# Performance work log

Hardware: AMD Instinct MI355X
Metric: run time of the kernel (lower is better)

## Reference

```python
import jax, jax.numpy as jnp
import numpy as np

BIT = 8
QMAX = 2 ** (BIT - 1) - 1          # 127
QMIN = -(2 ** (BIT - 1))           # -128
BOUNDARY_RANGE = 0.005
EPS = 1e-5


def _quant_act_int8(x):
    # StatsQ per-tensor activation quantization: scale from (1 - boundary_range)
    # quantile of |x| (robust absmax), fake-quant with STE.
    amax = jnp.maximum(jnp.quantile(jnp.abs(x), 1.0 - BOUNDARY_RANGE), EPS)
    s = QMAX / amax
    q = jnp.clip(jnp.round(x * s), QMIN, QMAX) / s
    return x + jax.lax.stop_gradient(q - x)


def _quant_w_ternary(w):
    # BitNet-1.58-style per-tensor ternary weight quantization:
    # gamma = mean(|W|); W_q in {-1, 0, +1} * gamma; STE.
    gamma = jnp.mean(jnp.abs(w)) + EPS
    q = jnp.clip(jnp.round(w / gamma), -1.0, 1.0) * gamma
    return w + jax.lax.stop_gradient(q - w)


def _qlinear(x, w):
    # quantize activations (int8 fake-quant) and weights (ternary), then matmul
    xq = _quant_act_int8(x)
    wq = _quant_w_ternary(w)
    return jnp.einsum('btd,hd->bth', xq, wq)


def _layernorm(x, g, b):
    mu = jnp.mean(x, axis=-1, keepdims=True)
    var = jnp.mean(jnp.square(x - mu), axis=-1, keepdims=True)
    return (x - mu) * jax.lax.rsqrt(var + 1e-5) * g + b


def setup_inputs() -> dict:
    key = jax.random.key(0)
    k_x, k_w1, k_w2 = jax.random.split(key, 3)
    B, T, D, H = 64, 256, 1024, 4096
    x = jax.random.normal(k_x, (B, T, D), dtype=jnp.float32)
    ln_g = jnp.ones((D,), dtype=jnp.float32)
    ln_b = jnp.zeros((D,), dtype=jnp.float32)
    w1 = jax.random.normal(k_w1, (H, D), dtype=jnp.float32) * (1.0 / np.sqrt(D))
    w2 = jax.random.normal(k_w2, (D, H), dtype=jnp.float32) * (1.0 / np.sqrt(H))
    return {'x': x, 'ln_g': ln_g, 'ln_b': ln_b, 'w1': w1, 'w2': w2}


def reference(x, ln_g, ln_b, w1, w2):
    h = _layernorm(x, ln_g, ln_b)          # [B,T,D]
    h = _qlinear(h, w1)                    # [B,T,H]
    h = jax.nn.gelu(h, approximate=False)  # torch nn.GELU default = exact erf
    out = _qlinear(h, w2)                  # [B,T,D]
    return out
```

## Files before the change

kernel.cpp:

```cpp
#include <hip/hip_runtime.h>
#include <hip/hip_fp16.h>
#include <math.h>


#define M_ROWS 16384
#define D_DIM  1024
#define H_DIM  4096

typedef int i32x4 __attribute__((ext_vector_type(4)));
typedef int i32x16 __attribute__((ext_vector_type(16)));

#define AS1 __attribute__((address_space(1)))
#define AS3 __attribute__((address_space(3)))

__device__ __forceinline__ void load_lds16(const void* g, void* l) {
  __builtin_amdgcn_global_load_lds((const AS1 void*)g, (AS3 void*)l, 16, 0, 0);
}

__device__ __forceinline__ float block_sum256(float v, float* lds) {
#pragma unroll
  for (int o = 32; o > 0; o >>= 1) v += __shfl_down(v, o, 64);
  int t = threadIdx.x;
  __syncthreads();
  if ((t & 63) == 0) lds[t >> 6] = v;
  __syncthreads();
  return lds[0] + lds[1] + lds[2] + lds[3];
}

__global__ __launch_bounds__(256) void k_layernorm(
    const float* __restrict__ x, const float* __restrict__ g,
    const float* __restrict__ b, __half* __restrict__ out) {
  __shared__ float lds[4];
  int row = blockIdx.x, t = threadIdx.x;
  float4 v = ((const float4*)(x + (size_t)row * D_DIM))[t];
  float s = v.x + v.y + v.z + v.w;
  s = block_sum256(s, lds);
  float mu = s * (1.0f / D_DIM);
  float d0 = v.x - mu, d1 = v.y - mu, d2 = v.z - mu, d3 = v.w - mu;
  float ss = d0 * d0 + d1 * d1 + d2 * d2 + d3 * d3;
  ss = block_sum256(ss, lds);
  float inv = 1.0f / sqrtf(ss * (1.0f / D_DIM) + 1e-5f);
  float4 gg = ((const float4*)g)[t];
  float4 bb = ((const float4*)b)[t];
  __half2 p0 = __floats2half2_rn(d0 * inv * gg.x + bb.x, d1 * inv * gg.y + bb.y);
  __half2 p1 = __floats2half2_rn(d2 * inv * gg.z + bb.z, d3 * inv * gg.w + bb.w);
  uint2 st;
  st.x = *(unsigned*)&p0;
  st.y = *(unsigned*)&p1;
  ((uint2*)(out + (size_t)row * D_DIM))[t] = st;
}

__global__ __launch_bounds__(256) void k_absmean2(const float4* __restrict__ w1,
                                                  const float4* __restrict__ w2,
                                                  size_t n4, double* __restrict__ out) {
  int which = (blockIdx.x >= (gridDim.x >> 1)) ? 1 : 0;
  const float4* p = which ? w2 : w1;
  unsigned half_grid = gridDim.x >> 1;
  unsigned blk = blockIdx.x - which * half_grid;
  double s = 0.0;
  size_t stride = (size_t)half_grid * blockDim.x;
  for (size_t i = (size_t)blk * blockDim.x + threadIdx.x; i < n4; i += stride) {
    float4 v = p[i];
    s += (double)fabsf(v.x) + (double)fabsf(v.y) + (double)fabsf(v.z) + (double)fabsf(v.w);
  }
#pragma unroll
  for (int o = 32; o > 0; o >>= 1) s += __shfl_down(s, o, 64);
  __shared__ double ds[4];
  int t = threadIdx.x;
  if ((t & 63) == 0) ds[t >> 6] = s;
  __syncthreads();
  if (t == 0) atomicAdd(out + which, ds[0] + ds[1] + ds[2] + ds[3]);
}

__device__ __forceinline__ int tern1(float w, float gamma) {
  return (int)fminf(1.f, fmaxf(-1.f, rintf(w / gamma)));
}

__global__ __launch_bounds__(256) void k_wquant2(const float4* __restrict__ w1,
                                                 const float4* __restrict__ w2,
                                                 unsigned* __restrict__ q1,
                                                 unsigned* __restrict__ q2, size_t n4,
                                                 const double* __restrict__ sump,
                                                 double inv_n, float* __restrict__ gamma_out) {
  int which = (blockIdx.x >= (gridDim.x >> 1)) ? 1 : 0;
  const float4* w = which ? w2 : w1;
  unsigned* wq = which ? q2 : q1;
  unsigned half_grid = gridDim.x >> 1;
  unsigned blk = blockIdx.x - which * half_grid;
  float gamma = (float)(sump[which] * inv_n) + 1e-5f;
  if (blk == 0 && threadIdx.x == 0) gamma_out[which] = gamma;
  size_t stride = (size_t)half_grid * blockDim.x;
  for (size_t i = (size_t)blk * blockDim.x + threadIdx.x; i < n4; i += stride) {
    float4 v = w[i];
    int a = tern1(v.x, gamma), b = tern1(v.y, gamma), c = tern1(v.z, gamma), d = tern1(v.w, gamma);
    wq[i] = (unsigned)(a & 255) | ((unsigned)(b & 255) << 8) |
            ((unsigned)(c & 255) << 16) | ((unsigned)(d & 255) << 24);
  }
}

__global__ __launch_bounds__(512) void k_hist16(const uint4* __restrict__ p, size_t n8,
                                                unsigned* __restrict__ hist) {
  extern __shared__ unsigned h[];
  int t = threadIdx.x;
  for (int i = t; i < 32768; i += 512) h[i] = 0;
  __syncthreads();
  size_t stride = (size_t)gridDim.x * 512;
  for (size_t i = (size_t)blockIdx.x * 512 + t; i < n8; i += stride) {
    uint4 u = p[i];
    atomicAdd(&h[u.x & 0x7FFFu], 1u);
    atomicAdd(&h[(u.x >> 16) & 0x7FFFu], 1u);
    atomicAdd(&h[u.y & 0x7FFFu], 1u);
    atomicAdd(&h[(u.y >> 16) & 0x7FFFu], 1u);
    atomicAdd(&h[u.z & 0x7FFFu], 1u);
    atomicAdd(&h[(u.z >> 16) & 0x7FFFu], 1u);
    atomicAdd(&h[u.w & 0x7FFFu], 1u);
    atomicAdd(&h[(u.w >> 16) & 0x7FFFu], 1u);
  }
  __syncthreads();
  for (int i = t; i < 32768; i += 512) {
    unsigned c = h[i];
    if (c) atomicAdd(&hist[i], c);
  }
}

__global__ __launch_bounds__(256) void k_scanq(const unsigned* __restrict__ hist,
                                               float* __restrict__ scl,
                                               unsigned long long k, double frac) {
  __shared__ unsigned tsum[256];
  __shared__ unsigned long long pre[256];
  __shared__ unsigned vk, vk1;
  int t = threadIdx.x;
  unsigned s = 0;
  for (int j = 0; j < 128; ++j) s += hist[t * 128 + j];
  tsum[t] = s;
  __syncthreads();
  if (t == 0) {
    unsigned long long c = 0;
    for (int i = 0; i < 256; ++i) { pre[i] = c; c += tsum[i]; }
  }
  __syncthreads();
  unsigned long long base = pre[t];
  for (int j = 0; j < 128; ++j) {
    unsigned c = hist[t * 128 + j];
    if (base <= k && k < base + c) vk = t * 128 + j;
    if (base <= k + 1 && k + 1 < base + c) vk1 = t * 128 + j;
    base += c;
  }
  __syncthreads();
  if (t == 0) {
    double a = (double)__half2float(__ushort_as_half((unsigned short)vk));
    double b = (double)__half2float(__ushort_as_half((unsigned short)vk1));
    double qv = (frac >= 0.5) ? (b - (b - a) * (1.0 - frac)) : (a + (b - a) * frac);
    float amax = fmaxf((float)qv, 1e-5f);
    scl[0] = amax;
    scl[1] = 127.0f / amax;
  }
}

__device__ __forceinline__ void unpack8(uint4 u, float* f) {
  __half2 h;
  h = *(__half2*)&u.x; f[0] = __low2float(h); f[1] = __high2float(h);
  h = *(__half2*)&u.y; f[2] = __low2float(h); f[3] = __high2float(h);
  h = *(__half2*)&u.z; f[4] = __low2float(h); f[5] = __high2float(h);
  h = *(__half2*)&u.w; f[6] = __low2float(h); f[7] = __high2float(h);
}

__device__ __forceinline__ unsigned qpack4(float a, float b, float c, float d, float s) {
  int qa = (int)fminf(127.f, fmaxf(-128.f, rintf(a * s)));
  int qb = (int)fminf(127.f, fmaxf(-128.f, rintf(b * s)));
  int qc = (int)fminf(127.f, fmaxf(-128.f, rintf(c * s)));
  int qd = (int)fminf(127.f, fmaxf(-128.f, rintf(d * s)));
  return (unsigned)(qa & 255) | ((unsigned)(qb & 255) << 8) |
         ((unsigned)(qc & 255) << 16) | ((unsigned)(qd & 255) << 24);
}

__global__ __launch_bounds__(256) void k_quant16(const uint4* __restrict__ p,
                                                 uint2* __restrict__ q, size_t n8,
                                                 const float* __restrict__ scl) {
  float s = scl[1];
  size_t stride = (size_t)gridDim.x * blockDim.x;
  for (size_t i = (size_t)blockIdx.x * blockDim.x + threadIdx.x; i < n8; i += stride) {
    float f[8];
    unpack8(p[i], f);
    uint2 r;
    r.x = qpack4(f[0], f[1], f[2], f[3], s);
    r.y = qpack4(f[4], f[5], f[6], f[7], s);
    q[i] = r;
  }
}

__device__ __forceinline__ float gelu_fast(float v) {
  float a = fabsf(v) * 0.70710678118654752f;
  float t = __builtin_amdgcn_rcpf(fmaf(0.3275911f, a, 1.0f));
  float p = t * fmaf(t, fmaf(t, fmaf(t, fmaf(t, 1.061405429f, -1.453152027f),
                                     1.421413741f), -0.284496736f), 0.254829592f);
  float e = __expf(-a * a);
  float er = fmaf(-p, e, 1.0f);
  float erf_s = copysignf(er, v);
  return 0.5f * v * (1.0f + erf_s);
}

template <int K, bool GELU>
__global__ __launch_bounds__(256, 4) void k_gemm(const signed char* __restrict__ A,
                                                 const signed char* __restrict__ B,
                                                 int N, void* __restrict__ outp,
                                                 const float* __restrict__ gamma_p,
                                                 const float* __restrict__ scl) {
  __shared__ __align__(16) signed char As[16384];
  __shared__ __align__(16) signed char Bs[16384];
  const int t = threadIdx.x;
  const int l = t & 63;
  const int wv = t >> 6;
  const int wr = (wv >> 1) * 64, wc = (wv & 1) * 64;
  const int m0 = blockIdx.y * 128, n0 = blockIdx.x * 128;

  const signed char* ag[4]; const signed char* bg[4];
  signed char* al[4]; signed char* bl[4];
#pragma unroll
  for (int c = 0; c < 4; ++c) {
    int g = c * 256 + t;
    int r = g >> 3;
    int cg = (g & 7) ^ (r & 7);
    ag[c] = A + (size_t)(m0 + r) * K + cg * 16;
    bg[c] = B + (size_t)(n0 + r) * K + cg * 16;
    al[c] = As + g * 16;
    bl[c] = Bs + g * 16;
  }

  int a_off[2][4], b_off[2][4];
#pragma unroll
  for (int mi = 0; mi < 2; ++mi)
#pragma unroll
    for (int ks = 0; ks < 4; ++ks) {
      int am = wr + mi * 32 + (l & 31);
      int g = 2 * ks + (l >> 5);
      a_off[mi][ks] = am * 128 + (g ^ (am & 7)) * 16;
      int bn = wc + mi * 32 + (l & 31);
      b_off[mi][ks] = bn * 128 + (g ^ (bn & 7)) * 16;
    }

  i32x16 acc[2][2];
#pragma unroll
  for (int mi = 0; mi < 2; ++mi)
#pragma unroll
    for (int ni = 0; ni < 2; ++ni)
      acc[mi][ni] = (i32x16)(0);

  for (int kk = 0; kk < K; kk += 512) {
#pragma unroll
    for (int j = 0; j < 4; ++j) {
      const int ko = j * 128;
      __syncthreads();
#pragma unroll
      for (int c = 0; c < 4; ++c) {
        load_lds16(ag[c] + kk + ko, al[c]);
        load_lds16(bg[c] + kk + ko, bl[c]);
      }
      __syncthreads();
#pragma unroll
      for (int ks = 0; ks < 4; ++ks) {
        i32x4 af[2], bf[2];
#pragma unroll
        for (int i = 0; i < 2; ++i) af[i] = *(const i32x4*)(As + a_off[i][ks]);
#pragma unroll
        for (int i = 0; i < 2; ++i) bf[i] = *(const i32x4*)(Bs + b_off[i][ks]);
#pragma unroll
        for (int mi = 0; mi < 2; ++mi)
#pragma unroll
          for (int ni = 0; ni < 2; ++ni)
            acc[mi][ni] = __builtin_amdgcn_mfma_i32_32x32x32_i8(af[mi], bf[ni], acc[mi][ni], 0, 0, 0);
      }
    }
  }

  const float cs = (*gamma_p) / scl[1];
  const int col0 = n0 + wc + (l & 31);
  const int row0 = m0 + wr + 4 * (l >> 5);
#pragma unroll
  for (int mi = 0; mi < 2; ++mi) {
#pragma unroll
    for (int ni = 0; ni < 2; ++ni) {
      int col = col0 + ni * 32;
#pragma unroll
      for (int reg = 0; reg < 16; ++reg) {
        int row = row0 + mi * 32 + (reg & 3) + 8 * (reg >> 2);
        float v = cs * (float)acc[mi][ni][reg];
        size_t idx = (size_t)row * N + col;
        if (GELU) {
          ((__half*)outp)[idx] = __float2half(gelu_fast(v));
        } else {
          ((float*)outp)[idx] = v;
        }
      }
    }
  }
}

extern "C" void kernel_launch(void* const* d_in, const int* in_sizes, int n_in,
                              void* d_out, int out_size, void* d_ws, size_t ws_size,
                              hipStream_t stream) {
  const float* x = (const float*)d_in[0];
  const float* ln_g = (const float*)d_in[1];
  const float* ln_b = (const float*)d_in[2];
  const float* w1 = (const float*)d_in[3];
  const float* w2 = (const float*)d_in[4];
  float* out = (float*)d_out;

  char* ws = (char*)d_ws;
  __half* h2 = (__half*)ws;
  __half* h1 = (__half*)(ws + ((size_t)128 << 20));
  signed char* xq1 = (signed char*)(ws + ((size_t)160 << 20));
  signed char* xq2 = (signed char*)(ws + ((size_t)128 << 20));
  signed char* w1q = (signed char*)(ws + ((size_t)192 << 20));
  signed char* w2q = (signed char*)(ws + ((size_t)196 << 20));
  char* sm = ws + ((size_t)200 << 20);
  unsigned* hista = (unsigned*)sm;
  unsigned* histb = (unsigned*)(sm + (128 << 10));
  double* wsum = (double*)(sm + (256 << 10));
  float* gamma = (float*)(sm + (256 << 10) + 16);
  float* scl1 = (float*)(sm + (256 << 10) + 32);
  float* scl2 = (float*)(sm + (256 << 10) + 40);

  hipMemsetAsync(sm, 0, (256 << 10) + 64, stream);
  hipFuncSetAttribute((const void*)k_hist16, hipFuncAttributeMaxDynamicSharedMemorySize,
                      131072);

  const double qq = 1.0 - 0.005;
  const unsigned long long N1 = (unsigned long long)M_ROWS * D_DIM;
  const unsigned long long N2 = (unsigned long long)M_ROWS * H_DIM;
  double idx1 = qq * (double)(N1 - 1);
  double idx2 = qq * (double)(N2 - 1);
  unsigned long long k1 = (unsigned long long)idx1;
  unsigned long long k2 = (unsigned long long)idx2;
  double frac1 = idx1 - (double)k1;
  double frac2 = idx2 - (double)k2;

  const size_t nW4 = (size_t)H_DIM * D_DIM / 4;
  const double inv_nW = 1.0 / (double)(H_DIM * D_DIM);

  k_absmean2<<<1024, 256, 0, stream>>>((const float4*)w1, (const float4*)w2, nW4, wsum);
  k_wquant2<<<2048, 256, 0, stream>>>((const float4*)w1, (const float4*)w2,
                                      (unsigned*)w1q, (unsigned*)w2q, nW4, wsum, inv_nW, gamma);

  k_layernorm<<<M_ROWS, 256, 0, stream>>>(x, ln_g, ln_b, h1);

  const size_t n8_1 = N1 / 8;
  k_hist16<<<256, 512, 131072, stream>>>((const uint4*)h1, n8_1, hista);
  k_scanq<<<1, 256, 0, stream>>>(hista, scl1, k1, frac1);
  k_quant16<<<1024, 256, 0, stream>>>((const uint4*)h1, (uint2*)xq1, n8_1, scl1);

  k_gemm<D_DIM, true><<<dim3(H_DIM / 128, M_ROWS / 128), 256, 0, stream>>>(
      xq1, w1q, H_DIM, (void*)h2, gamma + 0, scl1);

  const size_t n8_2 = N2 / 8;
  k_hist16<<<256, 512, 131072, stream>>>((const uint4*)h2, n8_2, histb);
  k_scanq<<<1, 256, 0, stream>>>(histb, scl2, k2, frac2);
  k_quant16<<<2048, 256, 0, stream>>>((const uint4*)h2, (uint2*)xq2, n8_2, scl2);

  k_gemm<H_DIM, false><<<dim3(D_DIM / 128, M_ROWS / 128), 256, 0, stream>>>(
      xq2, w2q, D_DIM, (void*)out, gamma + 1, scl2);
}
```

Measured before the change: 479.8 us.

## Register-prefetch GEMM tiles with smaller K-step and widen histogram blocks

The int8 GEMM drops the direct global-to-LDS loads of 128-wide K slices and stages 64-wide K slices through registers instead. The next slice's global load is issued before computing on the current one, so memory latency overlaps with MFMA work, and the LDS layout changes to a rotated-row scheme to avoid bank conflicts. The halved LDS footprint may allow higher occupancy, but the kernel now does twice as many barrier pairs per K and uses more VGPRs for the prefetch. The histogram kernel also moves to 1024-thread blocks.

```diff
diff --git a/kernel.cpp b/kernel.cpp
--- a/kernel.cpp
+++ b/kernel.cpp
@@ -9,13 +9,6 @@
 
 typedef int i32x4 __attribute__((ext_vector_type(4)));
 typedef int i32x16 __attribute__((ext_vector_type(16)));
-
-#define AS1 __attribute__((address_space(1)))
-#define AS3 __attribute__((address_space(3)))
-
-__device__ __forceinline__ void load_lds16(const void* g, void* l) {
-  __builtin_amdgcn_global_load_lds((const AS1 void*)g, (AS3 void*)l, 16, 0, 0);
-}
 
 __device__ __forceinline__ float block_sum256(float v, float* lds) {
 #pragma unroll
@@ -98,14 +91,14 @@
   }
 }
 
-__global__ __launch_bounds__(512) void k_hist16(const uint4* __restrict__ p, size_t n8,
-                                                unsigned* __restrict__ hist) {
+__global__ __launch_bounds__(1024) void k_hist16(const uint4* __restrict__ p, size_t n8,
+                                                 unsigned* __restrict__ hist) {
   extern __shared__ unsigned h[];
   int t = threadIdx.x;
-  for (int i = t; i < 32768; i += 512) h[i] = 0;
-  __syncthreads();
-  size_t stride = (size_t)gridDim.x * 512;
-  for (size_t i = (size_t)blockIdx.x * 512 + t; i < n8; i += stride) {
+  for (int i = t; i < 32768; i += 1024) h[i] = 0;
+  __syncthreads();
+  size_t stride = (size_t)gridDim.x * 1024;
+  for (size_t i = (size_t)blockIdx.x * 1024 + t; i < n8; i += stride) {
     uint4 u = p[i];
     atomicAdd(&h[u.x & 0x7FFFu], 1u);
     atomicAdd(&h[(u.x >> 16) & 0x7FFFu], 1u);
@@ -117,7 +110,7 @@
     atomicAdd(&h[(u.w >> 16) & 0x7FFFu], 1u);
   }
   __syncthreads();
-  for (int i = t; i < 32768; i += 512) {
+  for (int i = t; i < 32768; i += 1024) {
     unsigned c = h[i];
     if (c) atomicAdd(&hist[i], c);
   }
@@ -206,37 +199,35 @@
                                                  int N, void* __restrict__ outp,
                                                  const float* __restrict__ gamma_p,
                                                  const float* __restrict__ scl) {
-  __shared__ __align__(16) signed char As[16384];
-  __shared__ __align__(16) signed char Bs[16384];
+  __shared__ __align__(16) signed char As[8192];
+  __shared__ __align__(16) signed char Bs[8192];
   const int t = threadIdx.x;
   const int l = t & 63;
   const int wv = t >> 6;
   const int wr = (wv >> 1) * 64, wc = (wv & 1) * 64;
   const int m0 = blockIdx.y * 128, n0 = blockIdx.x * 128;
 
-  const signed char* ag[4]; const signed char* bg[4];
-  signed char* al[4]; signed char* bl[4];
-#pragma unroll
-  for (int c = 0; c < 4; ++c) {
-    int g = c * 256 + t;
-    int r = g >> 3;
-    int cg = (g & 7) ^ (r & 7);
-    ag[c] = A + (size_t)(m0 + r) * K + cg * 16;
-    bg[c] = B + (size_t)(n0 + r) * K + cg * 16;
-    al[c] = As + g * 16;
-    bl[c] = Bs + g * 16;
-  }
-
-  int a_off[2][4], b_off[2][4];
-#pragma unroll
-  for (int mi = 0; mi < 2; ++mi)
-#pragma unroll
-    for (int ks = 0; ks < 4; ++ks) {
-      int am = wr + mi * 32 + (l & 31);
+  const signed char* ga[2]; const signed char* gb[2];
+  int lw[2];
+#pragma unroll
+  for (int p = 0; p < 2; ++p) {
+    int s = p * 256 + t;
+    int row = s >> 2, g = s & 3;
+    ga[p] = A + (size_t)(m0 + row) * K + g * 16;
+    gb[p] = B + (size_t)(n0 + row) * K + g * 16;
+    lw[p] = g * 2048 + (((row + 2 * g) & 127) << 4);
+  }
+
+  int a_off[2][2], b_off[2][2];
+#pragma unroll
+  for (int i = 0; i < 2; ++i)
+#pragma unroll
+    for (int ks = 0; ks < 2; ++ks) {
       int g = 2 * ks + (l >> 5);
-      a_off[mi][ks] = am * 128 + (g ^ (am & 7)) * 16;
-      int bn = wc + mi * 32 + (l & 31);
-      b_off[mi][ks] = bn * 128 + (g ^ (bn & 7)) * 16;
+      int am = wr + i * 32 + (l & 31);
+      a_off[i][ks] = g * 2048 + (((am + 2 * g) & 127) << 4);
+      int bn = wc + i * 32 + (l & 31);
+      b_off[i][ks] = g * 2048 + (((bn + 2 * g) & 127) << 4);
     }
 
   i32x16 acc[2][2];
@@ -246,32 +237,48 @@
     for (int ni = 0; ni < 2; ++ni)
       acc[mi][ni] = (i32x16)(0);
 
-  for (int kk = 0; kk < K; kk += 512) {
-#pragma unroll
-    for (int j = 0; j < 4; ++j) {
-      const int ko = j * 128;
-      __syncthreads();
-#pragma unroll
-      for (int c = 0; c < 4; ++c) {
-        load_lds16(ag[c] + kk + ko, al[c]);
-        load_lds16(bg[c] + kk + ko, bl[c]);
-      }
-      __syncthreads();
-#pragma unroll
-      for (int ks = 0; ks < 4; ++ks) {
-        i32x4 af[2], bf[2];
-#pragma unroll
-        for (int i = 0; i < 2; ++i) af[i] = *(const i32x4*)(As + a_off[i][ks]);
-#pragma unroll
-        for (int i = 0; i < 2; ++i) bf[i] = *(const i32x4*)(Bs + b_off[i][ks]);
-#pragma unroll
-        for (int mi = 0; mi < 2; ++mi)
-#pragma unroll
-          for (int ni = 0; ni < 2; ++ni)
-            acc[mi][ni] = __builtin_amdgcn_mfma_i32_32x32x32_i8(af[mi], bf[ni], acc[mi][ni], 0, 0, 0);
-      }
+  uint4 pa0, pa1, pb0, pb1;
+  pa0 = *(const uint4*)(ga[0]);
+  pa1 = *(const uint4*)(ga[1]);
+  pb0 = *(const uint4*)(gb[0]);
+  pb1 = *(const uint4*)(gb[1]);
+
+  auto compute = [&]() {
+#pragma unroll
+    for (int ks = 0; ks < 2; ++ks) {
+      i32x4 af[2], bf[2];
+#pragma unroll
+      for (int i = 0; i < 2; ++i) af[i] = *(const i32x4*)(As + a_off[i][ks]);
+#pragma unroll
+      for (int i = 0; i < 2; ++i) bf[i] = *(const i32x4*)(Bs + b_off[i][ks]);
+#pragma unroll
+      for (int mi = 0; mi < 2; ++mi)
+#pragma unroll
+        for (int ni = 0; ni < 2; ++ni)
+          acc[mi][ni] = __builtin_amdgcn_mfma_i32_32x32x32_i8(af[mi], bf[ni], acc[mi][ni], 0, 0, 0);
     }
-  }
+  };
+
+  for (int kk = 0; kk < K - 64; kk += 64) {
+    __syncthreads();
+    *(uint4*)(As + lw[0]) = pa0;
+    *(uint4*)(As + lw[1]) = pa1;
+    *(uint4*)(Bs + lw[0]) = pb0;
+    *(uint4*)(Bs + lw[1]) = pb1;
+    pa0 = *(const uint4*)(ga[0] + kk + 64);
+    pa1 = *(const uint4*)(ga[1] + kk + 64);
+    pb0 = *(const uint4*)(gb[0] + kk + 64);
+    pb1 = *(const uint4*)(gb[1] + kk + 64);
+    __syncthreads();
+    compute();
+  }
+  __syncthreads();
+  *(uint4*)(As + lw[0]) = pa0;
+  *(uint4*)(As + lw[1]) = pa1;
+  *(uint4*)(Bs + lw[0]) = pb0;
+  *(uint4*)(Bs + lw[1]) = pb1;
+  __syncthreads();
+  compute();
 
   const float cs = (*gamma_p) / scl[1];
   const int col0 = n0 + wc + (l & 31);
@@ -345,7 +352,7 @@
   k_layernorm<<<M_ROWS, 256, 0, stream>>>(x, ln_g, ln_b, h1);
 
   const size_t n8_1 = N1 / 8;
-  k_hist16<<<256, 512, 131072, stream>>>((const uint4*)h1, n8_1, hista);
+  k_hist16<<<256, 1024, 131072, stream>>>((const uint4*)h1, n8_1, hista);
   k_scanq<<<1, 256, 0, stream>>>(hista, scl1, k1, frac1);
   k_quant16<<<1024, 256, 0, stream>>>((const uint4*)h1, (uint2*)xq1, n8_1, scl1);
 
@@ -353,7 +360,7 @@
       xq1, w1q, H_DIM, (void*)h2, gamma + 0, scl1);
 
   const size_t n8_2 = N2 / 8;
-  k_hist16<<<256, 512, 131072, stream>>>((const uint4*)h2, n8_2, histb);
+  k_hist16<<<256, 1024, 131072, stream>>>((const uint4*)h2, n8_2, histb);
   k_scanq<<<1, 256, 0, stream>>>(histb, scl2, k2, frac2);
   k_quant16<<<2048, 256, 0, stream>>>((const uint4*)h2, (uint2*)xq2, n8_2, scl2);
 
```

After: 507.3 us. +5.7%, slower.
